# Optimization experiments

Measured on AMD Instinct MI355X. Metric: run time of the kernel, lower is better.

The kernel has to match this reference:

```python
import jax, jax.numpy as jnp
import numpy as np

HID = 1152      # vision_hidden_size
HEADS = 16      # vision_num_heads
HD = HID // HEADS  # 72
INTER = 4304    # vision_intermediate_size
SEQ = 16384     # total vision tokens
WIN = 64        # tokens per attention window
EPS = 1e-6


def setup_inputs() -> dict:
    key = jax.random.key(0)
    ks = jax.random.split(key, 14)
    f32 = jnp.float32
    x = jax.random.normal(ks[0], (SEQ, HID), f32)
    # RoPE tables: standard rotary angles, full head_dim via concat(ang, ang)
    inv_freq = 1.0 / (10000.0 ** (jnp.arange(0, HD // 2, dtype=f32) / (HD // 2)))
    ang = jnp.arange(SEQ, dtype=f32)[:, None] * inv_freq[None, :]
    emb = jnp.concatenate([ang, ang], axis=-1)          # [SEQ, HD]
    cos, sin = jnp.cos(emb), jnp.sin(emb)
    cu_seqlens = jnp.arange(SEQ // WIN + 1, dtype=jnp.int32) * WIN  # uniform windows
    sc = 0.02
    return {
        "x": x, "cos": cos, "sin": sin, "cu_seqlens": cu_seqlens,
        "qkv_w": jax.random.normal(ks[1], (HID, 3 * HID), f32) * sc,
        "qkv_b": jnp.zeros((3 * HID,), f32),
        "proj_w": jax.random.normal(ks[2], (HID, HID), f32) * sc,
        "proj_b": jnp.zeros((HID,), f32),
        "ln1_w": jnp.ones((HID,), f32), "ln1_b": jnp.zeros((HID,), f32),
        "ln2_w": jnp.ones((HID,), f32), "ln2_b": jnp.zeros((HID,), f32),
        "fc1_w": jax.random.normal(ks[3], (HID, INTER), f32) * sc,
        "fc1_b": jnp.zeros((INTER,), f32),
        "fc2_w": jax.random.normal(ks[4], (INTER, HID), f32) * sc,
        "fc2_b": jnp.zeros((HID,), f32),
    }


def _layer_norm(h, w, b):
    hf = h.astype(jnp.float32)
    mean = jnp.mean(hf, axis=-1, keepdims=True)
    var = jnp.mean((hf - mean) ** 2, axis=-1, keepdims=True)
    return ((hf - mean) * jax.lax.rsqrt(var + EPS)) * w + b


def _rotate_half(t):
    t1, t2 = jnp.split(t, 2, axis=-1)
    return jnp.concatenate((-t2, t1), axis=-1)


def reference(x, cos, sin, cu_seqlens,
              qkv_w, qkv_b, proj_w, proj_b,
              ln1_w, ln1_b, ln2_w, ln2_b,
              fc1_w, fc1_b, fc2_w, fc2_b):
    S = x.shape[0]
    n_win = cu_seqlens.shape[0] - 1
    W = S // n_win  # uniform windows (block-diagonal attention)

    # --- attention branch ---
    h = _layer_norm(x, ln1_w, ln1_b)
    qkv = h @ qkv_w + qkv_b
    q, k, v = jnp.split(qkv, 3, axis=-1)
    q = q.reshape(S, HEADS, HD)
    k = k.reshape(S, HEADS, HD)
    v = v.reshape(S, HEADS, HD)
    c = cos[:, None, :HD]
    s = sin[:, None, :HD]
    q = q * c + _rotate_half(q) * s
    k = k * c + _rotate_half(k) * s
    # block-diagonal windowed attention: [n_win, W, HEADS, HD]
    qw = q.reshape(n_win, W, HEADS, HD).astype(jnp.float32)
    kw = k.reshape(n_win, W, HEADS, HD).astype(jnp.float32)
    vw = v.reshape(n_win, W, HEADS, HD).astype(jnp.float32)
    scores = jnp.einsum('wqhd,wkhd->whqk', qw, kw) * (HD ** -0.5)
    probs = jax.nn.softmax(scores, axis=-1)
    out = jnp.einsum('whqk,wkhd->wqhd', probs, vw).reshape(S, HID)
    x = x + (out @ proj_w + proj_b)

    # --- MLP branch ---
    h2 = _layer_norm(x, ln2_w, ln2_b)
    m = jax.nn.gelu(h2 @ fc1_w + fc1_b, approximate=True)
    return x + (m @ fc2_w + fc2_b)
```

## Files before the change

kernel.cpp:

```cpp
#include <hip/hip_runtime.h>
#include <stdint.h>


#define SEQ   16384
#define HID   1152
#define NH    16
#define HDIM  72
#define INTER 4304
#define INTERP 4352
#define QKVN  3456

using bf16x8 = __attribute__((ext_vector_type(8))) __bf16;
using f32x4  = __attribute__((ext_vector_type(4))) float;

__device__ __forceinline__ float bf2f(uint16_t u){ return __uint_as_float(((uint32_t)u)<<16); }
__device__ __forceinline__ uint16_t f2bf(float f){
  uint32_t u = __float_as_uint(f);
  u += 0x7fffu + ((u>>16)&1u);
  return (uint16_t)(u>>16);
}
__device__ __forceinline__ float gelu_fast(float x){
  const float z = 2.3022085f * x * (1.0f + 0.044715f*x*x);
  return x / (1.0f + exp2f(-z));
}
__device__ __forceinline__ void async_load16(const void* g, void* l){
  __builtin_amdgcn_global_load_lds((__attribute__((address_space(1))) void*)(void*)g,
                                   (__attribute__((address_space(3))) void*)l, 16, 0, 0);
}

__global__ void transpose_cast_all(const float* __restrict__ s0, uint16_t* __restrict__ d0,
                                   const float* __restrict__ s1, uint16_t* __restrict__ d1,
                                   const float* __restrict__ s2, uint16_t* __restrict__ d2,
                                   const float* __restrict__ s3, uint16_t* __restrict__ d3)
{
  __shared__ float tile[32][33];
  int b = blockIdx.x;
  const float* src; uint16_t* dst; int R, C, Rp, bx, by;
  if (b < 3888){        src = s0; dst = d0; R = 1152; C = 3456; Rp = 1152; bx = b % 108; by = b / 108; }
  else if (b < 5184){   b -= 3888; src = s1; dst = d1; R = 1152; C = 1152; Rp = 1152; bx = b % 36; by = b / 36; }
  else if (b < 10080){  b -= 5184; src = s2; dst = d2; R = 1152; C = 4304; Rp = 1152; bx = b % 136; by = b / 136; }
  else {                b -= 10080; src = s3; dst = d3; R = 4304; C = 1152; Rp = 4352; bx = b % 36; by = b / 36; }
  const int tx = threadIdx.x & 31, ty = threadIdx.x >> 5;
  const int c = bx*32 + tx;
  #pragma unroll
  for (int s = 0; s < 4; ++s){
    const int r = by*32 + ty + s*8;
    tile[ty + s*8][tx] = (r < R && c < C) ? src[(size_t)r*C + c] : 0.0f;
  }
  __syncthreads();
  #pragma unroll
  for (int s = 0; s < 4; ++s){
    const int oc = bx*32 + ty + s*8;
    const int orr = by*32 + tx;
    dst[(size_t)oc*Rp + orr] = f2bf(tile[tx][ty + s*8]);
  }
}

__global__ void ln_kernel(const float* __restrict__ x, const float* __restrict__ w,
                          const float* __restrict__ b, uint16_t* __restrict__ out)
{
  const int wid = threadIdx.x >> 6, lane = threadIdx.x & 63;
  const int row = blockIdx.x*4 + wid;
  const float2* xr = (const float2*)(x + (size_t)row*HID);
  float2 v[9];
  float s = 0.f;
  #pragma unroll
  for (int t = 0; t < 9; ++t){ v[t] = xr[lane + t*64]; s += v[t].x + v[t].y; }
  #pragma unroll
  for (int m = 32; m; m >>= 1) s += __shfl_xor(s, m, 64);
  const float mean = s * (1.0f/HID);
  float q = 0.f;
  #pragma unroll
  for (int t = 0; t < 9; ++t){
    float dx = v[t].x-mean, dy = v[t].y-mean;
    q += dx*dx + dy*dy;
  }
  #pragma unroll
  for (int m = 32; m; m >>= 1) q += __shfl_xor(q, m, 64);
  const float rstd = rsqrtf(q*(1.0f/HID) + 1e-6f);
  const float2* w2 = (const float2*)w;
  const float2* b2 = (const float2*)b;
  uint32_t* orow = (uint32_t*)(out + (size_t)row*HID);
  #pragma unroll
  for (int t = 0; t < 9; ++t){
    const int j = lane + t*64;
    const float2 wv = w2[j], bv = b2[j];
    const float o0 = (v[t].x-mean)*rstd*wv.x + bv.x;
    const float o1 = (v[t].y-mean)*rstd*wv.y + bv.y;
    orow[j] = (uint32_t)f2bf(o0) | ((uint32_t)f2bf(o1)<<16);
  }
}

__global__ __launch_bounds__(256,2) void attn_kernel(const uint16_t* __restrict__ qkv,
                                                     const float* __restrict__ cosb,
                                                     const float* __restrict__ sinb,
                                                     uint16_t* __restrict__ outb)
{
  __shared__ float Q[64*76];
  __shared__ float K[64*76];
  __shared__ float V[64*76];
  __shared__ float P[64*68];
  const int tid = threadIdx.x;
  const int win = blockIdx.x >> 4, h = blockIdx.x & 15;
  const size_t base = (size_t)win*64*QKVN + h*HDIM;
  {
    const int r = tid >> 2, q4 = tid & 3;
    const size_t rb = base + (size_t)r*QKVN;
    const float* crow = cosb + (size_t)(win*64 + r)*HDIM;
    const float* srow = sinb + (size_t)(win*64 + r)*HDIM;
    const int isK = q4 >> 1;
    const size_t mb = rb + (size_t)(isK ? HID : 0);
    float* dst = isK ? &K[r*76] : &Q[r*76];
    const int pb = (q4 & 1)*9;
    #pragma unroll
    for (int p0 = 0; p0 < 9; ++p0){
      const int d0 = (pb + p0)*2;
      const uint32_t ulo = *(const uint32_t*)(qkv + mb + d0);
      const uint32_t uhi = *(const uint32_t*)(qkv + mb + d0 + 36);
      const float2 c2 = *(const float2*)(crow + d0);
      const float2 s2 = *(const float2*)(srow + d0);
      const float l0 = bf2f((uint16_t)ulo), l1 = bf2f((uint16_t)(ulo>>16));
      const float h0 = bf2f((uint16_t)uhi), h1 = bf2f((uint16_t)(uhi>>16));
      dst[d0]    = l0*c2.x - h0*s2.x;
      dst[d0+1]  = l1*c2.y - h1*s2.y;
      dst[d0+36] = h0*c2.x + l0*s2.x;
      dst[d0+37] = h1*c2.y + l1*s2.y;
    }
    #pragma unroll
    for (int p0 = 0; p0 < 9; ++p0){
      const int p = q4*9 + p0;
      const uint32_t uv = *(const uint32_t*)(qkv + rb + 2*HID + 2*p);
      V[r*76+2*p] = bf2f((uint16_t)uv); V[r*76+2*p+1] = bf2f((uint16_t)(uv>>16));
    }
  }
  __syncthreads();
  const int rg = tid >> 4, cg = tid & 15;
  const int r0 = rg*4, c0 = cg*4;
  float sc[4][4] = {};
  #pragma unroll 3
  for (int kk = 0; kk < 18; ++kk){
    float4 qv[4], kv[4];
    #pragma unroll
    for (int i = 0; i < 4; ++i) qv[i] = *(const float4*)&Q[(r0+i)*76 + kk*4];
    #pragma unroll
    for (int j = 0; j < 4; ++j) kv[j] = *(const float4*)&K[(c0+j)*76 + kk*4];
    #pragma unroll
    for (int i = 0; i < 4; ++i)
      #pragma unroll
      for (int j = 0; j < 4; ++j)
        sc[i][j] += qv[i].x*kv[j].x + qv[i].y*kv[j].y + qv[i].z*kv[j].z + qv[i].w*kv[j].w;
  }
  const float scale = 0.11785113019775793f;
  #pragma unroll
  for (int i = 0; i < 4; ++i){
    float a0 = sc[i][0]*scale, a1 = sc[i][1]*scale, a2 = sc[i][2]*scale, a3 = sc[i][3]*scale;
    float m = fmaxf(fmaxf(a0,a1), fmaxf(a2,a3));
    m = fmaxf(m, __shfl_xor(m, 1, 16));
    m = fmaxf(m, __shfl_xor(m, 2, 16));
    m = fmaxf(m, __shfl_xor(m, 4, 16));
    m = fmaxf(m, __shfl_xor(m, 8, 16));
    float e0 = __expf(a0-m), e1 = __expf(a1-m), e2 = __expf(a2-m), e3 = __expf(a3-m);
    float sm = e0+e1+e2+e3;
    sm += __shfl_xor(sm, 1, 16);
    sm += __shfl_xor(sm, 2, 16);
    sm += __shfl_xor(sm, 4, 16);
    sm += __shfl_xor(sm, 8, 16);
    const float inv = 1.0f/sm;
    *(float4*)&P[(r0+i)*68 + c0] = make_float4(e0*inv, e1*inv, e2*inv, e3*inv);
  }
  __syncthreads();
  for (int d4 = cg; d4 < 18; d4 += 16){
    float4 o[4] = {};
    #pragma unroll 4
    for (int k4 = 0; k4 < 16; ++k4){
      float4 pr[4];
      #pragma unroll
      for (int i = 0; i < 4; ++i) pr[i] = *(const float4*)&P[(r0+i)*68 + k4*4];
      const float4 v0 = *(const float4*)&V[(k4*4+0)*76 + d4*4];
      const float4 v1 = *(const float4*)&V[(k4*4+1)*76 + d4*4];
      const float4 v2 = *(const float4*)&V[(k4*4+2)*76 + d4*4];
      const float4 v3 = *(const float4*)&V[(k4*4+3)*76 + d4*4];
      #pragma unroll
      for (int i = 0; i < 4; ++i){
        o[i].x += pr[i].x*v0.x + pr[i].y*v1.x + pr[i].z*v2.x + pr[i].w*v3.x;
        o[i].y += pr[i].x*v0.y + pr[i].y*v1.y + pr[i].z*v2.y + pr[i].w*v3.y;
        o[i].z += pr[i].x*v0.z + pr[i].y*v1.z + pr[i].z*v2.z + pr[i].w*v3.z;
        o[i].w += pr[i].x*v0.w + pr[i].y*v1.w + pr[i].z*v2.w + pr[i].w*v3.w;
      }
    }
    #pragma unroll
    for (int i = 0; i < 4; ++i){
      const int token = win*64 + r0 + i;
      const size_t ob = (size_t)token*HID + h*HDIM + d4*4;
      outb[ob+0] = f2bf(o[i].x); outb[ob+1] = f2bf(o[i].y);
      outb[ob+2] = f2bf(o[i].z); outb[ob+3] = f2bf(o[i].w);
    }
  }
}

template<int EPI, int NWJ>
__global__ __launch_bounds__(256,3) void gemm_bt(
    const uint16_t* __restrict__ A, const uint16_t* __restrict__ Bt,
    const float* __restrict__ bias, int Nb,
    const float* res, void* outp, int N, int K, int NB)
{
  __shared__ uint16_t sA[128*64];
  __shared__ uint16_t sB[32*NWJ*64];
  const int tid = threadIdx.x, wid = tid >> 6, lane = tid & 63;
  const int per  = gridDim.x >> 3;
  const int tile = (blockIdx.x & 7)*per + (blockIdx.x >> 3);
  const int mb   = tile / NB;
  const int mBase = mb*128, nBase = (tile - mb*NB)*(32*NWJ);
  const int wm = wid >> 1, wn = wid & 1;
  const int sr = lane >> 2;
  const int sk = lane & 3;
  const int gk = sk ^ ((sr >> 1) & 3);
  const int rr = lane & 15;
  const int rq = lane >> 4;
  const int rp = rq ^ ((rr >> 1) & 3);
  f32x4 acc[4][NWJ] = {};

  for (int k0 = 0; k0 < K; k0 += 64){
    __syncthreads();
    #pragma unroll
    for (int j = 0; j < 4; ++j){
      const int c  = wid*4 + j;
      const int rc = c >> 1, h = c & 1;
      const size_t gcol = (size_t)(k0 + h*32 + gk*8);
      async_load16(A + (size_t)(mBase + rc*16 + sr)*K + gcol, &sA[c*512]);
    }
    #pragma unroll
    for (int j = 0; j < NWJ; ++j){
      const int c  = wid*NWJ + j;
      const int rc = c >> 1, h = c & 1;
      const size_t gcol = (size_t)(k0 + h*32 + gk*8);
      async_load16(Bt + (size_t)(nBase + rc*16 + sr)*K + gcol, &sB[c*512]);
    }
    __syncthreads();
    #pragma unroll
    for (int h = 0; h < 2; ++h){
      bf16x8 af[4], bfr[NWJ];
      #pragma unroll
      for (int i = 0; i < 4; ++i)
        af[i] = *(const bf16x8*)&sA[((wm*4 + i)*2 + h)*512 + rr*32 + rp*8];
      #pragma unroll
      for (int j = 0; j < NWJ; ++j)
        bfr[j] = *(const bf16x8*)&sB[((wn*NWJ + j)*2 + h)*512 + rr*32 + rp*8];
      #pragma unroll
      for (int i = 0; i < 4; ++i)
        #pragma unroll
        for (int j = 0; j < NWJ; ++j)
          acc[i][j] = __builtin_amdgcn_mfma_f32_16x16x32_bf16(af[i], bfr[j], acc[i][j], 0, 0, 0);
    }
  }

  const int rqd = (lane>>4)*4, cl = lane & 15;
  #pragma unroll
  for (int i = 0; i < 4; ++i){
    #pragma unroll
    for (int j = 0; j < NWJ; ++j){
      const int col = nBase + wn*(NWJ*16) + j*16 + cl;
      const float bv = (col < Nb) ? bias[col] : 0.0f;
      #pragma unroll
      for (int r = 0; r < 4; ++r){
        const int row = mBase + wm*64 + i*16 + rqd + r;
        const float v = acc[i][j][r] + bv;
        const size_t o = (size_t)row*N + col;
        if (EPI == 0)      ((uint16_t*)outp)[o] = f2bf(v);
        else if (EPI == 1) ((uint16_t*)outp)[o] = f2bf(gelu_fast(v));
        else               ((float*)outp)[o] = v + res[o];
      }
    }
  }
}

extern "C" void kernel_launch(void* const* d_in, const int* in_sizes, int n_in,
                              void* d_out, int out_size, void* d_ws, size_t ws_size,
                              hipStream_t stream)
{
  const float* x      = (const float*)d_in[0];
  const float* cosb   = (const float*)d_in[1];
  const float* sinb   = (const float*)d_in[2];
  const float* qkv_w  = (const float*)d_in[4];
  const float* qkv_b  = (const float*)d_in[5];
  const float* proj_w = (const float*)d_in[6];
  const float* proj_b = (const float*)d_in[7];
  const float* ln1_w  = (const float*)d_in[8];
  const float* ln1_b  = (const float*)d_in[9];
  const float* ln2_w  = (const float*)d_in[10];
  const float* ln2_b  = (const float*)d_in[11];
  const float* fc1_w  = (const float*)d_in[12];
  const float* fc1_b  = (const float*)d_in[13];
  const float* fc2_w  = (const float*)d_in[14];
  const float* fc2_b  = (const float*)d_in[15];

  char* ws = (char*)d_ws;
  uint16_t* Wqkv  = (uint16_t*)(ws + 0);
  uint16_t* Wproj = (uint16_t*)(ws + 7962624);
  uint16_t* Wfc1  = (uint16_t*)(ws + 10616832);
  uint16_t* Wfc2  = (uint16_t*)(ws + 20643840);
  uint16_t* Hbuf  = (uint16_t*)(ws + 30670848);
  uint16_t* QKV   = (uint16_t*)(ws + 68419584);
  uint16_t* MB    = QKV;
  float* X1 = (float*)d_out;

  transpose_cast_all<<<14976, 256, 0, stream>>>(qkv_w, Wqkv, proj_w, Wproj,
                                                fc1_w, Wfc1, fc2_w, Wfc2);

  ln_kernel<<<4096, 256, 0, stream>>>(x, ln1_w, ln1_b, Hbuf);
  gemm_bt<0,3><<<36*128, 256, 0, stream>>>(Hbuf, Wqkv, qkv_b, QKVN, nullptr, QKV, QKVN, HID, 36);
  attn_kernel<<<4096, 256, 0, stream>>>(QKV, cosb, sinb, Hbuf);
  gemm_bt<2,3><<<12*128, 256, 0, stream>>>(Hbuf, Wproj, proj_b, HID, x, X1, HID, HID, 12);
  ln_kernel<<<4096, 256, 0, stream>>>(X1, ln2_w, ln2_b, Hbuf);
  gemm_bt<1,4><<<34*128, 256, 0, stream>>>(Hbuf, Wfc1, fc1_b, INTER, nullptr, MB, INTERP, HID, 34);
  gemm_bt<2,3><<<12*128, 256, 0, stream>>>(MB, Wfc2, fc2_b, HID, X1, X1, HID, INTERP, 12);
}
```

Measured before the change: 1.073 ms.

## Use bf16 MFMA for windowed attention QK and PV products

After: 1.000 ms. 6.8% less time.

```diff
diff --git a/kernel.cpp b/kernel.cpp
--- a/kernel.cpp
+++ b/kernel.cpp
@@ -19,6 +19,7 @@
   u += 0x7fffu + ((u>>16)&1u);
   return (uint16_t)(u>>16);
 }
+__device__ __forceinline__ uint32_t pk2(uint16_t a, uint16_t b){ return (uint32_t)a | ((uint32_t)b<<16); }
 __device__ __forceinline__ float gelu_fast(float x){
   const float z = 2.3022085f * x * (1.0f + 0.044715f*x*x);
   return x / (1.0f + exp2f(-z));
@@ -91,15 +92,15 @@
   }
 }
 
-__global__ __launch_bounds__(256,2) void attn_kernel(const uint16_t* __restrict__ qkv,
+__global__ __launch_bounds__(256,3) void attn_kernel(const uint16_t* __restrict__ qkv,
                                                      const float* __restrict__ cosb,
                                                      const float* __restrict__ sinb,
                                                      uint16_t* __restrict__ outb)
 {
-  __shared__ float Q[64*76];
-  __shared__ float K[64*76];
-  __shared__ float V[64*76];
-  __shared__ float P[64*68];
+  __shared__ uint16_t Qb[64*104];
+  __shared__ uint16_t Kb[64*104];
+  __shared__ uint16_t Vt[80*72];
+  __shared__ uint16_t Pb[64*72];
   const int tid = threadIdx.x;
   const int win = blockIdx.x >> 4, h = blockIdx.x & 15;
   const size_t base = (size_t)win*64*QKVN + h*HDIM;
@@ -110,7 +111,7 @@
     const float* srow = sinb + (size_t)(win*64 + r)*HDIM;
     const int isK = q4 >> 1;
     const size_t mb = rb + (size_t)(isK ? HID : 0);
-    float* dst = isK ? &K[r*76] : &Q[r*76];
+    uint16_t* dst = isK ? &Kb[r*104] : &Qb[r*104];
     const int pb = (q4 & 1)*9;
     #pragma unroll
     for (int p0 = 0; p0 < 9; ++p0){
@@ -121,39 +122,42 @@
       const float2 s2 = *(const float2*)(srow + d0);
       const float l0 = bf2f((uint16_t)ulo), l1 = bf2f((uint16_t)(ulo>>16));
       const float h0 = bf2f((uint16_t)uhi), h1 = bf2f((uint16_t)(uhi>>16));
-      dst[d0]    = l0*c2.x - h0*s2.x;
-      dst[d0+1]  = l1*c2.y - h1*s2.y;
-      dst[d0+36] = h0*c2.x + l0*s2.x;
-      dst[d0+37] = h1*c2.y + l1*s2.y;
-    }
+      *(uint32_t*)&dst[d0]    = pk2(f2bf(l0*c2.x - h0*s2.x), f2bf(l1*c2.y - h1*s2.y));
+      *(uint32_t*)&dst[d0+36] = pk2(f2bf(h0*c2.x + l0*s2.x), f2bf(h1*c2.y + l1*s2.y));
+    }
+    const int zb = (q4 & 1)*6;
+    #pragma unroll
+    for (int z = 0; z < 6; ++z) *(uint32_t*)&dst[72 + (zb + z)*2] = 0;
     #pragma unroll
     for (int p0 = 0; p0 < 9; ++p0){
       const int p = q4*9 + p0;
       const uint32_t uv = *(const uint32_t*)(qkv + rb + 2*HID + 2*p);
-      V[r*76+2*p] = bf2f((uint16_t)uv); V[r*76+2*p+1] = bf2f((uint16_t)(uv>>16));
-    }
+      Vt[(2*p+0)*72 + r] = (uint16_t)uv;
+      Vt[(2*p+1)*72 + r] = (uint16_t)(uv>>16);
+    }
+  }
+  {
+    const int d = 72 + (tid >> 5), t = (tid & 31)*2;
+    *(uint32_t*)&Vt[d*72 + t] = 0;
   }
   __syncthreads();
-  const int rg = tid >> 4, cg = tid & 15;
-  const int r0 = rg*4, c0 = cg*4;
-  float sc[4][4] = {};
-  #pragma unroll 3
-  for (int kk = 0; kk < 18; ++kk){
-    float4 qv[4], kv[4];
-    #pragma unroll
-    for (int i = 0; i < 4; ++i) qv[i] = *(const float4*)&Q[(r0+i)*76 + kk*4];
-    #pragma unroll
-    for (int j = 0; j < 4; ++j) kv[j] = *(const float4*)&K[(c0+j)*76 + kk*4];
-    #pragma unroll
-    for (int i = 0; i < 4; ++i)
-      #pragma unroll
-      for (int j = 0; j < 4; ++j)
-        sc[i][j] += qv[i].x*kv[j].x + qv[i].y*kv[j].y + qv[i].z*kv[j].z + qv[i].w*kv[j].w;
+
+  const int wv = tid >> 6, lane = tid & 63;
+  const int fr = lane & 15, fq = lane >> 4;
+  f32x4 sacc[4] = {};
+  #pragma unroll
+  for (int ks = 0; ks < 3; ++ks){
+    const bf16x8 aq = *(const bf16x8*)&Qb[(wv*16 + fr)*104 + ks*32 + fq*8];
+    #pragma unroll
+    for (int j = 0; j < 4; ++j){
+      const bf16x8 bk = *(const bf16x8*)&Kb[(j*16 + fr)*104 + ks*32 + fq*8];
+      sacc[j] = __builtin_amdgcn_mfma_f32_16x16x32_bf16(aq, bk, sacc[j], 0, 0, 0);
+    }
   }
   const float scale = 0.11785113019775793f;
   #pragma unroll
-  for (int i = 0; i < 4; ++i){
-    float a0 = sc[i][0]*scale, a1 = sc[i][1]*scale, a2 = sc[i][2]*scale, a3 = sc[i][3]*scale;
+  for (int r = 0; r < 4; ++r){
+    float a0 = sacc[0][r]*scale, a1 = sacc[1][r]*scale, a2 = sacc[2][r]*scale, a3 = sacc[3][r]*scale;
     float m = fmaxf(fmaxf(a0,a1), fmaxf(a2,a3));
     m = fmaxf(m, __shfl_xor(m, 1, 16));
     m = fmaxf(m, __shfl_xor(m, 2, 16));
@@ -166,34 +170,31 @@
     sm += __shfl_xor(sm, 4, 16);
     sm += __shfl_xor(sm, 8, 16);
     const float inv = 1.0f/sm;
-    *(float4*)&P[(r0+i)*68 + c0] = make_float4(e0*inv, e1*inv, e2*inv, e3*inv);
-  }
-  __syncthreads();
-  for (int d4 = cg; d4 < 18; d4 += 16){
-    float4 o[4] = {};
-    #pragma unroll 4
-    for (int k4 = 0; k4 < 16; ++k4){
-      float4 pr[4];
-      #pragma unroll
-      for (int i = 0; i < 4; ++i) pr[i] = *(const float4*)&P[(r0+i)*68 + k4*4];
-      const float4 v0 = *(const float4*)&V[(k4*4+0)*76 + d4*4];
-      const float4 v1 = *(const float4*)&V[(k4*4+1)*76 + d4*4];
-      const float4 v2 = *(const float4*)&V[(k4*4+2)*76 + d4*4];
-      const float4 v3 = *(const float4*)&V[(k4*4+3)*76 + d4*4];
-      #pragma unroll
-      for (int i = 0; i < 4; ++i){
-        o[i].x += pr[i].x*v0.x + pr[i].y*v1.x + pr[i].z*v2.x + pr[i].w*v3.x;
-        o[i].y += pr[i].x*v0.y + pr[i].y*v1.y + pr[i].z*v2.y + pr[i].w*v3.y;
-        o[i].z += pr[i].x*v0.z + pr[i].y*v1.z + pr[i].z*v2.z + pr[i].w*v3.z;
-        o[i].w += pr[i].x*v0.w + pr[i].y*v1.w + pr[i].z*v2.w + pr[i].w*v3.w;
+    const int prow = wv*16 + fq*4 + r;
+    Pb[prow*72 +  0 + fr] = f2bf(e0*inv);
+    Pb[prow*72 + 16 + fr] = f2bf(e1*inv);
+    Pb[prow*72 + 32 + fr] = f2bf(e2*inv);
+    Pb[prow*72 + 48 + fr] = f2bf(e3*inv);
+  }
+  f32x4 oacc[5] = {};
+  #pragma unroll
+  for (int k2 = 0; k2 < 2; ++k2){
+    const bf16x8 ap = *(const bf16x8*)&Pb[(wv*16 + fr)*72 + k2*32 + fq*8];
+    #pragma unroll
+    for (int j = 0; j < 5; ++j){
+      const bf16x8 bv = *(const bf16x8*)&Vt[(j*16 + fr)*72 + k2*32 + fq*8];
+      oacc[j] = __builtin_amdgcn_mfma_f32_16x16x32_bf16(ap, bv, oacc[j], 0, 0, 0);
+    }
+  }
+  #pragma unroll
+  for (int j = 0; j < 5; ++j){
+    const int d = j*16 + fr;
+    if (d < HDIM){
+      #pragma unroll
+      for (int r = 0; r < 4; ++r){
+        const int token = win*64 + wv*16 + fq*4 + r;
+        outb[(size_t)token*HID + h*HDIM + d] = f2bf(oacc[j][r]);
       }
-    }
-    #pragma unroll
-    for (int i = 0; i < 4; ++i){
-      const int token = win*64 + r0 + i;
-      const size_t ob = (size_t)token*HID + h*HDIM + d4*4;
-      outb[ob+0] = f2bf(o[i].x); outb[ob+1] = f2bf(o[i].y);
-      outb[ob+2] = f2bf(o[i].z); outb[ob+3] = f2bf(o[i].w);
     }
   }
 }
```
